# Kernel optimization log

Hardware: AMD Instinct MI355X
Metric: run time of the kernel (lower is better)

Reference implementation:

```python
import jax, jax.numpy as jnp
import numpy as np

C_LEN, Q_LEN, D = 8192, 1024, 1024  # D = 2*hidden_size


def setup_inputs() -> dict:
    key = jax.random.key(0)
    ks = jax.random.split(key, 5)
    scale = 1.0 / np.sqrt(D)
    return {
        "H": jax.random.normal(ks[0], (C_LEN, D), dtype=jnp.float32),
        "U": jax.random.normal(ks[1], (Q_LEN, D), dtype=jnp.float32),
        "w_q": jax.random.normal(ks[2], (D,), dtype=jnp.float32) * scale,
        "b_q": jnp.zeros((1,), dtype=jnp.float32),
        "w_c": jax.random.normal(ks[3], (D,), dtype=jnp.float32) * scale,
        "b_c": jnp.zeros((1,), dtype=jnp.float32),
        "w_qc": jax.random.normal(ks[4], (D,), dtype=jnp.float32) * scale,
        "b_qc": jnp.zeros((1,), dtype=jnp.float32),
    }


def reference(H, U, w_q, b_q, w_c, b_c, w_qc, b_qc):
    # Per-token loop qc[:, i] = (H * U[i]) @ w_qc + b_qc collapses to one GEMM:
    # qc[j, i] = sum_k H[j,k] * w_qc[k] * U[i,k] + b_qc
    qc = jnp.einsum("cd,qd->cq", H * w_qc, U) + b_qc          # [c_len, q_len]
    q_term = (U @ w_q + b_q)[None, :]                          # [1, q_len]
    c_term = (H @ w_c + b_c)[:, None]                          # [c_len, 1]
    s = qc + q_term + c_term                                    # [c_len, q_len]
    q2c_atten = jax.nn.softmax(s, axis=0)                       # softmax over context dim (as written)
    U_toggler = q2c_atten @ U                                   # [c_len, D]
    b = jnp.max(H, axis=1)                                      # [c_len]
    c2q_atten = jax.nn.softmax(b)                               # [c_len]
    H_toggler = jnp.broadcast_to((c2q_atten @ H)[None, :], (H.shape[0], H.shape[1]))
    return (U_toggler, H_toggler)
```

## Files before the change

kernel.cpp:

```cpp
#include <hip/hip_runtime.h>

#define C_LEN 8192
#define Q_LEN 1024
#define DDIM  1024

typedef __attribute__((ext_vector_type(8))) short short8;
typedef __attribute__((ext_vector_type(4))) float f32x4;

static __device__ __forceinline__ unsigned short f2bf(float f){
  unsigned u = __float_as_uint(f);
  unsigned rounding = 0x7fffu + ((u >> 16) & 1u);
  return (unsigned short)((u + rounding) >> 16);
}

static __device__ __forceinline__ void async_copy16(const void* g, void* l){
  __builtin_amdgcn_global_load_lds(
      (const __attribute__((address_space(1))) void*)g,
      (__attribute__((address_space(3))) void*)l, 16, 0, 0);
}

static __device__ __forceinline__ float waveRedSum(float v){
  #pragma unroll
  for(int o=32;o;o>>=1) v += __shfl_down(v,o);
  return v;
}
static __device__ __forceinline__ float waveRedMax(float v){
  #pragma unroll
  for(int o=32;o;o>>=1) v = fmaxf(v,__shfl_down(v,o));
  return v;
}

__global__ void prep_HU(const float* __restrict__ H, const float* __restrict__ U,
                        const float* __restrict__ w_qc, const float* __restrict__ w_c,
                        const float* __restrict__ b_c, const float* __restrict__ w_q,
                        const float* __restrict__ b_q,
                        unsigned short* __restrict__ Abf, float* __restrict__ cterm,
                        float* __restrict__ eb, unsigned short* __restrict__ Ubf,
                        float* __restrict__ qterm, float* __restrict__ csum){
  const int b = blockIdx.x, t = threadIdx.x;
  __shared__ float sd[4], sm[4];
  const int w = t>>6, l = t&63;
  if(b < C_LEN){
    float4 h   = reinterpret_cast<const float4*>(H + (size_t)b*DDIM)[t];
    float4 wqc = reinterpret_cast<const float4*>(w_qc)[t];
    float4 wc  = reinterpret_cast<const float4*>(w_c)[t];
    float dot = h.x*wc.x + h.y*wc.y + h.z*wc.z + h.w*wc.w;
    float mx  = fmaxf(fmaxf(h.x,h.y), fmaxf(h.z,h.w));
    ushort4 o;
    o.x=f2bf(h.x*wqc.x); o.y=f2bf(h.y*wqc.y); o.z=f2bf(h.z*wqc.z); o.w=f2bf(h.w*wqc.w);
    reinterpret_cast<ushort4*>(Abf)[(size_t)b*256 + t] = o;
    dot = waveRedSum(dot); mx = waveRedMax(mx);
    if(l==0){ sd[w]=dot; sm[w]=mx; }
    __syncthreads();
    if(t==0){
      cterm[b] = sd[0]+sd[1]+sd[2]+sd[3] + b_c[0];
      float m = fmaxf(fmaxf(sm[0],sm[1]), fmaxf(sm[2],sm[3]));
      eb[b] = __expf(m);
    }
  } else {
    const int qr = b - C_LEN;
    float4 u  = reinterpret_cast<const float4*>(U + (size_t)qr*DDIM)[t];
    float4 wq = reinterpret_cast<const float4*>(w_q)[t];
    float dot = u.x*wq.x + u.y*wq.y + u.z*wq.z + u.w*wq.w;
    ushort4 o; o.x=f2bf(u.x); o.y=f2bf(u.y); o.z=f2bf(u.z); o.w=f2bf(u.w);
    reinterpret_cast<ushort4*>(Ubf)[(size_t)qr*256 + t] = o;
    dot = waveRedSum(dot);
    if(l==0) sd[w]=dot;
    __syncthreads();
    if(t==0){
      qterm[qr] = sd[0]+sd[1]+sd[2]+sd[3] + b_q[0];
      csum[qr]  = 0.f;
    }
  }
}

__global__ void h_weighted(const float* __restrict__ H, const float* __restrict__ eb,
                           float* __restrict__ Hpart){
  int d  = blockIdx.x*256 + threadIdx.x;
  int cb = blockIdx.y, c0 = cb*256;
  float acc = 0.f;
  for(int c=c0;c<c0+256;c++)
    acc += eb[c] * H[(size_t)c*DDIM + d];
  Hpart[cb*DDIM + d] = acc;
}

__global__ void combine_Hrow(const float* __restrict__ Hpart, const float* __restrict__ eb,
                             float* __restrict__ Hrow){
  __shared__ float red[4];
  int t = threadIdx.x, w = t>>6, l = t&63;
  float s = 0.f;
  for(int i=t;i<C_LEN;i+=256) s += eb[i];
  s = waveRedSum(s);
  if(!l) red[w] = s;
  __syncthreads();
  float btot = red[0]+red[1]+red[2]+red[3];
  int d = blockIdx.x*256 + t;
  float acc = 0.f;
  #pragma unroll
  for(int p=0;p<32;p++) acc += Hpart[p*DDIM + d];
  Hrow[d] = acc / btot;
}

__global__ void transpose_scale_U(const float* __restrict__ U, const float* __restrict__ csum,
                                  unsigned short* __restrict__ Ut){
  __shared__ float tile[64][65];
  const int t = threadIdx.x;
  const int q0 = blockIdx.y*64, d0 = blockIdx.x*64;
  #pragma unroll
  for(int i=0;i<16;i++){
    int idx = i*256 + t, r = idx>>6, col = idx&63;
    tile[r][col] = U[(size_t)(q0+r)*DDIM + d0 + col];
  }
  float inv = 1.f / csum[q0 + (t&63)];
  __syncthreads();
  #pragma unroll
  for(int i=0;i<16;i++){
    int idx = i*256 + t, r = idx>>6, col = idx&63;
    Ut[(size_t)(d0+r)*Q_LEN + q0 + col] = f2bf(tile[col][r] * inv);
  }
}

template<int FUSE_EXP>
__global__ __launch_bounds__(256)
void gemm_bt(const unsigned short* __restrict__ A, const unsigned short* __restrict__ B,
             void* __restrict__ Cout, int M, int N, int K,
             const float* __restrict__ rowAdd, const float* __restrict__ colAdd,
             const float* __restrict__ addC, float* __restrict__ csum,
             const float* __restrict__ Hrow, float* __restrict__ outH){
  __shared__ unsigned short As[2][128][32];
  __shared__ unsigned short Bs[2][128][32];
  const int t = threadIdx.x;
  const int lane = t & 63, wave = t >> 6;
  const int wm = wave & 1, wn = wave >> 1;
  const int lr = lane & 15, quad = lane >> 4;
  const int L = blockIdx.x + (blockIdx.y << 6);
  const int xcd = L & 7, r = L >> 3;
  const int by = r & 7, bx = ((r >> 3) << 3) | xcd;
  const int bm = bx * 128, bn = by * 128;
  const int srow = wave*32 + (lane>>2);
  const int skcol = (lane&3)*8;

  f32x4 acc[4][4];
  #pragma unroll
  for(int i=0;i<4;i++)
    #pragma unroll
    for(int j=0;j<4;j++) acc[i][j] = (f32x4){0.f,0.f,0.f,0.f};

  const unsigned short* gA = A + (size_t)(bm + srow)*K + skcol;
  const unsigned short* gB = B + (size_t)(bn + srow)*K + skcol;
  unsigned short* lA[2] = { &As[0][srow][skcol], &As[1][srow][skcol] };
  unsigned short* lB[2] = { &Bs[0][srow][skcol], &Bs[1][srow][skcol] };

  async_copy16(gA,                lA[0]);
  async_copy16(gA + (size_t)16*K, lA[0] + 16*32);
  async_copy16(gB,                lB[0]);
  async_copy16(gB + (size_t)16*K, lB[0] + 16*32);
  gA += 32; gB += 32;

  const int ITERS = K >> 5;
  for(int k=0;k<ITERS;k++){
    const int cur = k & 1, nxt = cur ^ 1;
    __syncthreads();
    if(k+1 < ITERS){
      async_copy16(gA,                lA[nxt]);
      async_copy16(gA + (size_t)16*K, lA[nxt] + 16*32);
      async_copy16(gB,                lB[nxt]);
      async_copy16(gB + (size_t)16*K, lB[nxt] + 16*32);
      gA += 32; gB += 32;
    }
    short8 af[4], bfr[4];
    #pragma unroll
    for(int i=0;i<4;i++){
      af[i]  = *reinterpret_cast<const short8*>(&As[cur][wm*64 + i*16 + lr][quad*8]);
      bfr[i] = *reinterpret_cast<const short8*>(&Bs[cur][wn*64 + i*16 + lr][quad*8]);
    }
    #pragma unroll
    for(int i=0;i<4;i++)
      #pragma unroll
      for(int j=0;j<4;j++)
        acc[i][j] = __builtin_amdgcn_mfma_f32_16x16x32_bf16(af[i], bfr[j], acc[i][j], 0,0,0);
  }

  const int col0 = bn + wn*64;
  if(FUSE_EXP){
    unsigned short* P = (unsigned short*)Cout;
    const float ac = addC[0];
    float cs[4];
    #pragma unroll
    for(int j=0;j<4;j++) cs[j] = 0.f;
    #pragma unroll
    for(int i=0;i<4;i++){
      int row0 = bm + wm*64 + i*16 + quad*4;
      float ra0 = rowAdd[row0], ra1 = rowAdd[row0+1], ra2 = rowAdd[row0+2], ra3 = rowAdd[row0+3];
      #pragma unroll
      for(int j=0;j<4;j++){
        int col = col0 + j*16 + lr;
        float cadd = colAdd[col] + ac;
        float e0 = __expf(acc[i][j][0] + ra0 + cadd);
        float e1 = __expf(acc[i][j][1] + ra1 + cadd);
        float e2 = __expf(acc[i][j][2] + ra2 + cadd);
        float e3 = __expf(acc[i][j][3] + ra3 + cadd);
        P[(size_t)(row0  )*N + col] = f2bf(e0);
        P[(size_t)(row0+1)*N + col] = f2bf(e1);
        P[(size_t)(row0+2)*N + col] = f2bf(e2);
        P[(size_t)(row0+3)*N + col] = f2bf(e3);
        cs[j] += e0+e1+e2+e3;
      }
    }
    #pragma unroll
    for(int j=0;j<4;j++){
      float v = cs[j];
      v += __shfl_xor(v, 16);
      v += __shfl_xor(v, 32);
      if(quad==0) atomicAdd(&csum[col0 + j*16 + lr], v);
    }
  } else {
    float* C = (float*)Cout;
    #pragma unroll
    for(int i=0;i<4;i++){
      int row0 = bm + wm*64 + i*16 + quad*4;
      #pragma unroll
      for(int j=0;j<4;j++){
        int col = col0 + j*16 + lr;
        #pragma unroll
        for(int r=0;r<4;r++)
          C[(size_t)(row0+r)*N + col] = acc[i][j][r];
      }
    }
    float4 hv = reinterpret_cast<const float4*>(Hrow + bn)[t & 31];
    #pragma unroll
    for(int rr = t>>5; rr < 128; rr += 8)
      reinterpret_cast<float4*>(outH + (size_t)(bm+rr)*DDIM + bn)[t & 31] = hv;
  }
}

extern "C" void kernel_launch(void* const* d_in, const int* in_sizes, int n_in,
                              void* d_out, int out_size, void* d_ws, size_t ws_size,
                              hipStream_t stream){
  const float* H    = (const float*)d_in[0];
  const float* U    = (const float*)d_in[1];
  const float* w_q  = (const float*)d_in[2];
  const float* b_q  = (const float*)d_in[3];
  const float* w_c  = (const float*)d_in[4];
  const float* b_c  = (const float*)d_in[5];
  const float* w_qc = (const float*)d_in[6];
  const float* b_qc = (const float*)d_in[7];
  float* out = (float*)d_out;
  char*  ws  = (char*)d_ws;

  unsigned short* P    = (unsigned short*)(ws);
  unsigned short* Abf  = (unsigned short*)(ws + 16777216);
  unsigned short* Ubf  = (unsigned short*)(ws + 33554432);
  unsigned short* Utb  = (unsigned short*)(ws + 35651584);
  char* stats = ws + 37748736;
  float* csum  = (float*)(stats);
  float* Hrow  = (float*)(stats + 4096);
  float* cterm = (float*)(stats + 12288);
  float* eb    = (float*)(stats + 45056);
  float* qterm = (float*)(stats + 77824);
  float* Hpart = (float*)(stats + 81920);

  prep_HU<<<C_LEN + Q_LEN, 256, 0, stream>>>(H, U, w_qc, w_c, b_c, w_q, b_q,
                                             Abf, cterm, eb, Ubf, qterm, csum);

  h_weighted  <<<dim3(4,32), 256, 0, stream>>>(H, eb, Hpart);
  combine_Hrow<<<4, 256, 0, stream>>>(Hpart, eb, Hrow);

  gemm_bt<1><<<dim3(64,8), 256, 0, stream>>>(Abf, Ubf, (void*)P, C_LEN, Q_LEN, DDIM,
                                             cterm, qterm, b_qc, csum, nullptr, nullptr);

  transpose_scale_U<<<dim3(16,16), 256, 0, stream>>>(U, csum, Utb);

  gemm_bt<0><<<dim3(64,8), 256, 0, stream>>>(P, Utb, (void*)out, C_LEN, DDIM, Q_LEN,
                                             nullptr, nullptr, nullptr, nullptr,
                                             Hrow, out + (size_t)C_LEN*DDIM);
}
```

Measured before the change: 176.4 us.

## Triple-buffer GEMM LDS loads with explicit waitcnt; split H-weighted reduction finer

Changes the bf16 MFMA GEMM main loop from a double-buffered to a triple-buffered async global-to-LDS pipeline. It prefetches two stages ahead and uses an explicit s_waitcnt on vmcnt plus s_barrier instead of __syncthreads, so loads overlap more with MFMA work. Separately, the h_weighted reduction is split into 128 chunks of 64 rows instead of 32 chunks of 256, giving more blocks, and combine_Hrow now sums 128 partials. In exchange, the GEMM uses more LDS, and the hand-coded waitcnt encodings carry a correctness risk if they do not match the number of loads in flight.

```diff
diff --git a/kernel.cpp b/kernel.cpp
--- a/kernel.cpp
+++ b/kernel.cpp
@@ -77,9 +77,9 @@
 __global__ void h_weighted(const float* __restrict__ H, const float* __restrict__ eb,
                            float* __restrict__ Hpart){
   int d  = blockIdx.x*256 + threadIdx.x;
-  int cb = blockIdx.y, c0 = cb*256;
+  int cb = blockIdx.y, c0 = cb*64;
   float acc = 0.f;
-  for(int c=c0;c<c0+256;c++)
+  for(int c=c0;c<c0+64;c++)
     acc += eb[c] * H[(size_t)c*DDIM + d];
   Hpart[cb*DDIM + d] = acc;
 }
@@ -97,7 +97,7 @@
   int d = blockIdx.x*256 + t;
   float acc = 0.f;
   #pragma unroll
-  for(int p=0;p<32;p++) acc += Hpart[p*DDIM + d];
+  for(int p=0;p<128;p++) acc += Hpart[p*DDIM + d];
   Hrow[d] = acc / btot;
 }
 
@@ -127,8 +127,8 @@
              const float* __restrict__ rowAdd, const float* __restrict__ colAdd,
              const float* __restrict__ addC, float* __restrict__ csum,
              const float* __restrict__ Hrow, float* __restrict__ outH){
-  __shared__ unsigned short As[2][128][32];
-  __shared__ unsigned short Bs[2][128][32];
+  __shared__ unsigned short As[3][128][32];
+  __shared__ unsigned short Bs[3][128][32];
   const int t = threadIdx.x;
   const int lane = t & 63, wave = t >> 6;
   const int wm = wave & 1, wn = wave >> 1;
@@ -148,38 +148,47 @@
 
   const unsigned short* gA = A + (size_t)(bm + srow)*K + skcol;
   const unsigned short* gB = B + (size_t)(bn + srow)*K + skcol;
-  unsigned short* lA[2] = { &As[0][srow][skcol], &As[1][srow][skcol] };
-  unsigned short* lB[2] = { &Bs[0][srow][skcol], &Bs[1][srow][skcol] };
-
-  async_copy16(gA,                lA[0]);
-  async_copy16(gA + (size_t)16*K, lA[0] + 16*32);
-  async_copy16(gB,                lB[0]);
-  async_copy16(gB + (size_t)16*K, lB[0] + 16*32);
-  gA += 32; gB += 32;
+  unsigned short* lA[3] = { &As[0][srow][skcol], &As[1][srow][skcol], &As[2][srow][skcol] };
+  unsigned short* lB[3] = { &Bs[0][srow][skcol], &Bs[1][srow][skcol], &Bs[2][srow][skcol] };
+
+  #define STAGE(batch, buf) do {                                         \
+    const unsigned short* _a = gA + (size_t)(batch)*32;                  \
+    const unsigned short* _b = gB + (size_t)(batch)*32;                  \
+    async_copy16(_a,                lA[buf]);                            \
+    async_copy16(_a + (size_t)16*K, lA[buf] + 16*32);                    \
+    async_copy16(_b,                lB[buf]);                            \
+    async_copy16(_b + (size_t)16*K, lB[buf] + 16*32);                    \
+  } while(0)
 
   const int ITERS = K >> 5;
+  STAGE(0, 0);
+  STAGE(1, 1);
+
+  int cb = 0;
   for(int k=0;k<ITERS;k++){
-    const int cur = k & 1, nxt = cur ^ 1;
-    __syncthreads();
-    if(k+1 < ITERS){
-      async_copy16(gA,                lA[nxt]);
-      async_copy16(gA + (size_t)16*K, lA[nxt] + 16*32);
-      async_copy16(gB,                lB[nxt]);
-      async_copy16(gB + (size_t)16*K, lB[nxt] + 16*32);
-      gA += 32; gB += 32;
+    if(k < ITERS-1) __builtin_amdgcn_s_waitcnt(0x0F74);
+    else            __builtin_amdgcn_s_waitcnt(0x0F70);
+    __builtin_amdgcn_s_barrier();
+    asm volatile("" ::: "memory");
+    if(k+2 < ITERS){
+      int nb = cb;
+      nb = cb + 2; if(nb >= 3) nb -= 3;
+      STAGE(k+2, nb);
     }
     short8 af[4], bfr[4];
     #pragma unroll
     for(int i=0;i<4;i++){
-      af[i]  = *reinterpret_cast<const short8*>(&As[cur][wm*64 + i*16 + lr][quad*8]);
-      bfr[i] = *reinterpret_cast<const short8*>(&Bs[cur][wn*64 + i*16 + lr][quad*8]);
+      af[i]  = *reinterpret_cast<const short8*>(&As[cb][wm*64 + i*16 + lr][quad*8]);
+      bfr[i] = *reinterpret_cast<const short8*>(&Bs[cb][wn*64 + i*16 + lr][quad*8]);
     }
     #pragma unroll
     for(int i=0;i<4;i++)
       #pragma unroll
       for(int j=0;j<4;j++)
         acc[i][j] = __builtin_amdgcn_mfma_f32_16x16x32_bf16(af[i], bfr[j], acc[i][j], 0,0,0);
-  }
+    cb = cb + 1; if(cb >= 3) cb = 0;
+  }
+  #undef STAGE
 
   const int col0 = bn + wn*64;
   if(FUSE_EXP){
@@ -223,8 +232,8 @@
       for(int j=0;j<4;j++){
         int col = col0 + j*16 + lr;
         #pragma unroll
-        for(int r=0;r<4;r++)
-          C[(size_t)(row0+r)*N + col] = acc[i][j][r];
+        for(int rr=0;rr<4;rr++)
+          C[(size_t)(row0+rr)*N + col] = acc[i][j][rr];
       }
     }
     float4 hv = reinterpret_cast<const float4*>(Hrow + bn)[t & 31];
@@ -263,7 +272,7 @@
   prep_HU<<<C_LEN + Q_LEN, 256, 0, stream>>>(H, U, w_qc, w_c, b_c, w_q, b_q,
                                              Abf, cterm, eb, Ubf, qterm, csum);
 
-  h_weighted  <<<dim3(4,32), 256, 0, stream>>>(H, eb, Hpart);
+  h_weighted  <<<dim3(4,128), 256, 0, stream>>>(H, eb, Hpart);
   combine_Hrow<<<4, 256, 0, stream>>>(Hpart, eb, Hrow);
 
   gemm_bt<1><<<dim3(64,8), 256, 0, stream>>>(Abf, Ubf, (void*)P, C_LEN, Q_LEN, DDIM,
```

Result: slower. 211.8 us (+20.1%).
